# Kernel tuning notes

Hardware: AMD Instinct MI355X
Metric: run time of the kernel (lower is better)

Reference implementation:

```python
import jax, jax.numpy as jnp
import numpy as np

N = 50000        # num nodes
E = 800000       # num edges (before self loops)
F_DIM = 256      # embedding_dim
H = 4            # num_heads
C = 64           # latent_dim
SLOPE = 0.2      # PyG GATConv leaky_relu negative_slope


def setup_inputs() -> dict:
    key = jax.random.key(0)
    ks = jax.random.split(key, 11)
    s = 0.05
    return {
        "x": jax.random.normal(ks[0], (N, F_DIM), jnp.float32),
        "edge_index": jax.random.randint(ks[1], (2, E), 0, N),
        "W1": jax.random.normal(ks[2], (F_DIM, H * C), jnp.float32) * s,
        "a_src1": jax.random.normal(ks[3], (H, C), jnp.float32) * s,
        "a_dst1": jax.random.normal(ks[4], (H, C), jnp.float32) * s,
        "b1": jnp.zeros((H * C,), jnp.float32),
        "W2": jax.random.normal(ks[5], (H * C, F_DIM), jnp.float32) * s,
        "a_src2": jax.random.normal(ks[6], (1, F_DIM), jnp.float32) * s,
        "a_dst2": jax.random.normal(ks[7], (1, F_DIM), jnp.float32) * s,
        "b2": jnp.zeros((F_DIM,), jnp.float32),
    }


def gat_layer(x, src, dst, W, a_src, a_dst, bias, heads, out_ch):
    n = x.shape[0]
    xW = (x @ W).reshape(n, heads, out_ch)              # [N,H,C]
    alpha_s = jnp.sum(xW * a_src, axis=-1)               # [N,H]
    alpha_d = jnp.sum(xW * a_dst, axis=-1)               # [N,H]
    e = jax.nn.leaky_relu(alpha_s[src] + alpha_d[dst], SLOPE)  # [E,H]
    m = jax.ops.segment_max(e, dst, num_segments=n)      # segment-softmax over in-edges
    w = jnp.exp(e - m[dst])
    z = jax.ops.segment_sum(w, dst, num_segments=n)
    alpha = w / z[dst]                                    # [E,H]
    out = jax.ops.segment_sum(xW[src] * alpha[:, :, None], dst, num_segments=n)  # [N,H,C]
    return out.reshape(n, heads * out_ch) + bias          # concat=True


def reference(x, edge_index, W1, a_src1, a_dst1, b1, W2, a_src2, a_dst2, b2):
    loop = jnp.arange(N)  # PyG default add_self_loops=True
    src = jnp.concatenate([edge_index[0], loop])
    dst = jnp.concatenate([edge_index[1], loop])
    h = jax.nn.elu(gat_layer(x, src, dst, W1, a_src1, a_dst1, b1, H, C))
    return gat_layer(h, src, dst, W2, a_src2, a_dst2, b2, 1, F_DIM)
```

## Files before the change

### kernel.cpp

```cpp
#include <hip/hip_runtime.h>
#include <hip/hip_bf16.h>
#include <math.h>

#define N_NODES 50000
#define N_EDGES 800000
#define ETOT    (N_EDGES + N_NODES)
#define FDIM    256
#define SLOPE   0.2f

typedef __bf16    bf16x8 __attribute__((ext_vector_type(8)));
typedef float     f32x4  __attribute__((ext_vector_type(4)));
typedef _Float16  f16x8  __attribute__((ext_vector_type(8)));
typedef _Float16  f16x4  __attribute__((ext_vector_type(4)));

__global__ void count_edges(const int* __restrict__ dst, int* __restrict__ counts) {
    int i = blockIdx.x * blockDim.x + threadIdx.x;
    if (i < N_EDGES) atomicAdd(&counts[dst[i]], 1);
}

__global__ void scan1(const int* __restrict__ counts, int* __restrict__ partial,
                      int* __restrict__ blockSums) {
    __shared__ int wsum[4];
    int b = blockIdx.x, t = threadIdx.x;
    int base = b * 1024;
    int i0 = base + t * 4;
    int v[4];
#pragma unroll
    for (int u = 0; u < 4; u++) { int i = i0 + u; v[u] = (i < N_NODES) ? (counts[i] + 1) : 0; }
    v[1] += v[0]; v[2] += v[1]; v[3] += v[2];
    int lane = t & 63, wid = t >> 6;
    int incl = v[3];
#pragma unroll
    for (int d = 1; d < 64; d <<= 1) {
        int o = __shfl_up(incl, d, 64);
        if (lane >= d) incl += o;
    }
    if (lane == 63) wsum[wid] = incl;
    __syncthreads();
    int woff = 0;
#pragma unroll
    for (int w = 0; w < 4; w++) if (w < wid) woff += wsum[w];
    int texcl = woff + incl - v[3];
#pragma unroll
    for (int u = 0; u < 4; u++) { int i = i0 + u; if (i < N_NODES) partial[i] = texcl + v[u]; }
    if (t == 255) blockSums[b] = woff + incl;
}

__global__ void scan3(const int* __restrict__ partial, const int* __restrict__ blockSums,
                      int* __restrict__ row_ptr, int* __restrict__ cursor) {
    int b = blockIdx.x, t = threadIdx.x;
    __shared__ int s_off;
    if (t < 64) {
        int v = (t < b) ? blockSums[t] : 0;
#pragma unroll
        for (int d = 1; d < 64; d <<= 1) v += __shfl_xor(v, d, 64);
        if (t == 0) s_off = v;
    }
    __syncthreads();
    int off = s_off;
    int base = b * 1024;
#pragma unroll
    for (int u = 0; u < 4; u++) {
        int i = base + t + u * 256;
        if (i < N_NODES) {
            row_ptr[i + 1] = off + partial[i];
            cursor[i]      = off + ((i == base) ? 0 : partial[i - 1]);
        }
    }
    if (b == 0 && t == 0) row_ptr[0] = 0;
}

__global__ void scatter_edges(const int* __restrict__ src, const int* __restrict__ dst,
                              int* __restrict__ cursor, int* __restrict__ col_src) {
    int i = blockIdx.x * blockDim.x + threadIdx.x;
    if (i >= ETOT) return;
    int s, d;
    if (i < N_EDGES) { s = src[i]; d = dst[i]; }
    else             { s = i - N_EDGES; d = s; }
    int p = atomicAdd(&cursor[d], 1);
    col_src[p] = s;
}

__global__ void pack_w2(const float* __restrict__ W1, const float* __restrict__ W2,
                        __bf16* __restrict__ P1, __bf16* __restrict__ P2) {
    int tid = blockIdx.x * 256 + threadIdx.x;
    const float* W = (tid < 65536) ? W1 : W2;
    __bf16* P = (tid < 65536) ? P1 : P2;
    int t = tid & 65535;
    int j    = t & 7;
    int lane = (t >> 3) & 63;
    int nb   = (t >> 9) & 3;
    int w    = (t >> 11) & 3;
    int step = (t >> 13) & 7;
    int col = (w << 6) | (nb << 4) | (lane & 15);
    int k   = (step << 5) | ((lane >> 4) << 3) | j;
    float v = W[(k << 8) | col];
    __bf16 h = (__bf16)v;
    int base = (((((step << 2) | w) << 2) | nb) << 10) | (lane << 3) | j;
    P[base]       = h;
    P[base + 512] = (__bf16)(v - (float)h);
}

template <int HEADS, typename AT>
__global__ __launch_bounds__(256) void gemm_mfma(
        const AT* __restrict__ A, const __bf16* __restrict__ Bpk,
        _Float16* __restrict__ Ch,
        const float* __restrict__ avS, const float* __restrict__ avD,
        float* __restrict__ aS, float* __restrict__ aD, int M) {
    constexpr int LDA = 40;
    constexpr int LDC = 272;
    __shared__ union SMem {
        struct { __bf16 Ah[2][64 * LDA]; __bf16 Al[2][64 * LDA]; } st;
        _Float16 cts[64][LDC];
    } smem;
    __shared__ float sred[2][64][4];

    const int t = threadIdx.x;
    const int w = t >> 6, l = t & 63;
    const int q = l >> 4, c16 = l & 15;
    const int row0 = blockIdx.x * 64;

    const int ar = t >> 2, ak = (t & 3) << 3;
    const bool arow_ok = (row0 + ar) < M;
    const AT* Arow = A + (size_t)(row0 + ar) * 256 + ak;

    f32x4 acc[4][4];
#pragma unroll
    for (int i = 0; i < 4; i++)
#pragma unroll
        for (int j = 0; j < 4; j++) acc[i][j] = (f32x4){0.f, 0.f, 0.f, 0.f};

    float4 pv0 = make_float4(0.f, 0.f, 0.f, 0.f), pv1 = pv0;
    f16x8  pvh = (f16x8){0, 0, 0, 0, 0, 0, 0, 0};
    if (arow_ok) {
        if constexpr (sizeof(AT) == 4) {
            pv0 = *(const float4*)(Arow);
            pv1 = *(const float4*)(Arow + 4);
        } else {
            pvh = *(const f16x8*)(Arow);
        }
    }

    for (int step = 0; step < 8; ++step) {
        const int k0 = step << 5;
        const int buf = step & 1;

        {
            float vv[8];
            if constexpr (sizeof(AT) == 4) {
                vv[0] = pv0.x; vv[1] = pv0.y; vv[2] = pv0.z; vv[3] = pv0.w;
                vv[4] = pv1.x; vv[5] = pv1.y; vv[6] = pv1.z; vv[7] = pv1.w;
            } else {
#pragma unroll
                for (int j = 0; j < 8; j++) vv[j] = (float)pvh[j];
            }
            bf16x8 hv, lv;
#pragma unroll
            for (int j = 0; j < 8; j++) {
                __bf16 hb = (__bf16)vv[j];
                hv[j] = hb;
                lv[j] = (__bf16)(vv[j] - (float)hb);
            }
            *(bf16x8*)(&smem.st.Ah[buf][ar * LDA + ak]) = hv;
            *(bf16x8*)(&smem.st.Al[buf][ar * LDA + ak]) = lv;
        }
        if (step < 7 && arow_ok) {
            if constexpr (sizeof(AT) == 4) {
                pv0 = *(const float4*)(Arow + k0 + 32);
                pv1 = *(const float4*)(Arow + k0 + 36);
            } else {
                pvh = *(const f16x8*)(Arow + k0 + 32);
            }
        }
        const __bf16* Bs = Bpk + ((size_t)((step << 2) | w) << 12);
        bf16x8 bh[4], bl[4];
#pragma unroll
        for (int nb = 0; nb < 4; nb++) {
            bh[nb] = *(const bf16x8*)(Bs + (nb << 10) + (l << 3));
            bl[nb] = *(const bf16x8*)(Bs + (nb << 10) + 512 + (l << 3));
        }
        __syncthreads();

        bf16x8 ah[4], alo[4];
#pragma unroll
        for (int mb = 0; mb < 4; mb++) {
            int off = (c16 + (mb << 4)) * LDA + (q << 3);
            ah[mb]  = *(const bf16x8*)(&smem.st.Ah[buf][off]);
            alo[mb] = *(const bf16x8*)(&smem.st.Al[buf][off]);
        }
#pragma unroll
        for (int mb = 0; mb < 4; mb++)
#pragma unroll
            for (int nb = 0; nb < 4; nb++) {
                acc[mb][nb] = __builtin_amdgcn_mfma_f32_16x16x32_bf16(ah[mb],  bh[nb], acc[mb][nb], 0, 0, 0);
                acc[mb][nb] = __builtin_amdgcn_mfma_f32_16x16x32_bf16(ah[mb],  bl[nb], acc[mb][nb], 0, 0, 0);
                acc[mb][nb] = __builtin_amdgcn_mfma_f32_16x16x32_bf16(alo[mb], bh[nb], acc[mb][nb], 0, 0, 0);
            }
    }
    __syncthreads();

#pragma unroll
    for (int mb = 0; mb < 4; mb++) {
#pragma unroll
        for (int r = 0; r < 4; r++) {
            int row = (mb << 4) + (q << 2) + r;
            float s = 0.f, d = 0.f;
#pragma unroll
            for (int nb = 0; nb < 4; nb++) {
                int col = (w << 6) + (nb << 4) + c16;
                float val = acc[mb][nb][r];
                s = fmaf(val, avS[col], s);
                d = fmaf(val, avD[col], d);
                smem.cts[row][col] = (_Float16)val;
            }
#pragma unroll
            for (int dd = 1; dd < 16; dd <<= 1) {
                s += __shfl_xor(s, dd, 64);
                d += __shfl_xor(d, dd, 64);
            }
            if (c16 == 0) { sred[0][row][w] = s; sred[1][row][w] = d; }
        }
    }
    __syncthreads();

    {
        const int crow = t >> 2;
        const int grow = row0 + crow;
        if (grow < M) {
            _Float16* dstp = Ch + (size_t)grow * 256;
#pragma unroll
            for (int i = 0; i < 8; i++) {
                int col = ((t & 3) << 3) + (i << 5);
                *(f16x8*)(dstp + col) = *(const f16x8*)(&smem.cts[crow][col]);
            }
        }
    }
    if (HEADS == 4) {
        int row = t >> 2, wv = t & 3;
        int v = row0 + row;
        if (v < M) { aS[v * 4 + wv] = sred[0][row][wv]; aD[v * 4 + wv] = sred[1][row][wv]; }
    } else {
        if (t < 64) {
            int v = row0 + t;
            if (v < M) {
                aS[v] = sred[0][t][0] + sred[0][t][1] + sred[0][t][2] + sred[0][t][3];
                aD[v] = sred[1][t][0] + sred[1][t][1] + sred[1][t][2] + sred[1][t][3];
            }
        }
    }
}

template <int HEADS, bool ELU, typename OT>
__global__ __launch_bounds__(256) void gat_aggregate_wave(
        const _Float16* __restrict__ xWh, const float* __restrict__ aS,
        const float* __restrict__ aD, const int* __restrict__ row_ptr,
        const int* __restrict__ col_src, const float* __restrict__ bias,
        OT* __restrict__ out) {
    const int wid  = threadIdx.x >> 6;
    const int lane = threadIdx.x & 63;
    const int v = blockIdx.x * 4 + wid;
    if (v >= N_NODES) return;

    constexpr int CH = 64 / HEADS;
    const int h = (HEADS == 4) ? (lane >> 4) : 0;
    const int q = (HEADS == 4) ? (lane & 15) : lane;

    const int half = lane >> 5;
    const int fl   = lane & 31;
    const int hf   = (HEADS == 4) ? (fl >> 3) : 0;
    const int wbase = (HEADS == 4) ? (hf << 4) : 0;

    const int beg = row_ptr[v], end = row_ptr[v + 1];
    const float adv = aD[v * HEADS + h];

    float acc[8] = {0.f, 0.f, 0.f, 0.f, 0.f, 0.f, 0.f, 0.f};
    float z = 0.f;
    for (int j0 = beg; j0 < end; j0 += CH) {
        const int cnt = min(CH, end - j0);
        int s = 0;
        float wgt = 0.f;
        if (q < cnt) {
            s = col_src[j0 + q];
            float e = aS[s * HEADS + h] + adv;
            e = (e > 0.f) ? e : SLOPE * e;
            wgt = __expf(e);
        }
        z += wgt;
        for (int jj = 0; jj < cnt; jj += 2) {
            const int qm = jj + half;
            const int sl = wbase | qm;
            const int   sj = __shfl(s,   sl, 64);
            const float wj = __shfl(wgt, sl, 64);
            if (qm < cnt) {
                const f16x8 row = *(const f16x8*)(xWh + ((size_t)sj << 8) + (fl << 3));
#pragma unroll
                for (int i = 0; i < 8; i++)
                    acc[i] = fmaf(wj, (float)row[i], acc[i]);
            }
        }
    }
#pragma unroll
    for (int d = 1; d < CH; d <<= 1) z += __shfl_xor(z, d, 64);
    const float zf = (HEADS == 4) ? __shfl(z, hf << 4, 64) : z;

#pragma unroll
    for (int i = 0; i < 8; i++) acc[i] += __shfl_xor(acc[i], 32, 64);

    const float rz = 1.f / zf;
    const int fbase = (fl << 3) + (half << 2);
    const float4 bv = *(const float4*)(bias + fbase);
    float4 o;
    o.x = acc[(half << 2) + 0] * rz + bv.x;
    o.y = acc[(half << 2) + 1] * rz + bv.y;
    o.z = acc[(half << 2) + 2] * rz + bv.z;
    o.w = acc[(half << 2) + 3] * rz + bv.w;
    if (ELU) {
        o.x = (o.x > 0.f) ? o.x : expm1f(o.x);
        o.y = (o.y > 0.f) ? o.y : expm1f(o.y);
        o.z = (o.z > 0.f) ? o.z : expm1f(o.z);
        o.w = (o.w > 0.f) ? o.w : expm1f(o.w);
    }
    if constexpr (sizeof(OT) == 2) {
        f16x4 ov;
        ov[0] = (_Float16)o.x; ov[1] = (_Float16)o.y;
        ov[2] = (_Float16)o.z; ov[3] = (_Float16)o.w;
        *(f16x4*)(out + ((size_t)v << 8) + fbase) = ov;
    } else {
        *(float4*)(out + ((size_t)v << 8) + fbase) = o;
    }
}

extern "C" void kernel_launch(void* const* d_in, const int* in_sizes, int n_in,
                              void* d_out, int out_size, void* d_ws, size_t ws_size,
                              hipStream_t stream) {
    const float* x   = (const float*)d_in[0];
    const int*   ei  = (const int*)d_in[1];
    const float* W1  = (const float*)d_in[2];
    const float* as1 = (const float*)d_in[3];
    const float* ad1 = (const float*)d_in[4];
    const float* b1  = (const float*)d_in[5];
    const float* W2  = (const float*)d_in[6];
    const float* as2 = (const float*)d_in[7];
    const float* ad2 = (const float*)d_in[8];
    const float* b2  = (const float*)d_in[9];
    float* out = (float*)d_out;

    const int* src = ei;
    const int* dst = ei + N_EDGES;

    char* w = (char*)d_ws;
    _Float16* xWh = (_Float16*)w; w += (size_t)N_NODES * 256 * 2;
    _Float16* hh  = (_Float16*)w; w += (size_t)N_NODES * 256 * 2;
    float* aS = (float*)w;  w += (size_t)N_NODES * 4 * 4;
    float* aD = (float*)w;  w += (size_t)N_NODES * 4 * 4;
    int* row_ptr = (int*)w; w += (((size_t)(N_NODES + 1) * 4 + 255) / 256) * 256;
    int* counts  = (int*)w; w += (((size_t)N_NODES * 4 + 255) / 256) * 256;
    int* cursor  = (int*)w; w += (((size_t)N_NODES * 4 + 255) / 256) * 256;
    int* partial = (int*)w; w += (((size_t)N_NODES * 4 + 255) / 256) * 256;
    int* bsums   = (int*)w; w += 256;
    int* col_src = (int*)w; w += (size_t)ETOT * 4;
    __bf16* Wpk1 = (__bf16*)w; w += 131072 * 2;
    __bf16* Wpk2 = (__bf16*)w; w += 131072 * 2;

    int nb = (N_NODES + 1023) / 1024;

    pack_w2<<<512, 256, 0, stream>>>(W1, W2, Wpk1, Wpk2);

    hipMemsetAsync(counts, 0, (size_t)N_NODES * 4, stream);
    count_edges<<<(N_EDGES + 255) / 256, 256, 0, stream>>>(dst, counts);
    scan1<<<nb, 256, 0, stream>>>(counts, partial, bsums);
    scan3<<<nb, 256, 0, stream>>>(partial, bsums, row_ptr, cursor);
    scatter_edges<<<(ETOT + 255) / 256, 256, 0, stream>>>(src, dst, cursor, col_src);

    int gemm_blocks = (N_NODES + 63) / 64;
    int agg_blocks  = (N_NODES + 3) / 4;

    gemm_mfma<4, float><<<gemm_blocks, 256, 0, stream>>>(x, Wpk1, xWh, as1, ad1, aS, aD, N_NODES);
    gat_aggregate_wave<4, true, _Float16><<<agg_blocks, 256, 0, stream>>>(xWh, aS, aD, row_ptr, col_src, b1, hh);

    gemm_mfma<1, _Float16><<<gemm_blocks, 256, 0, stream>>>(hh, Wpk2, xWh, as2, ad2, aS, aD, N_NODES);
    gat_aggregate_wave<1, false, float><<<agg_blocks, 256, 0, stream>>>(xWh, aS, aD, row_ptr, col_src, b2, out);
}
```

Baseline: 299.0 us.

## Fuse CSR build into one cooperative kernel and enlarge GEMM row tile

Replaces the memset, count, two scan and scatter launches with a single cooperative kernel that uses grid-wide syncs between phases, cutting launch overhead and inter-kernel gaps. Separately, the MFMA GEMM now processes 128 rows per block instead of 64, so each B fragment load is reused across twice as many rows. The epilogue is split into two halves so the existing 64-row shared staging buffer still works. Costs are more accumulator registers, possibly lower occupancy, grid.sync overhead, and only 512 blocks doing the atomic-heavy edge phases.

```diff
diff --git a/kernel.cpp b/kernel.cpp
--- a/kernel.cpp
+++ b/kernel.cpp
@@ -1,84 +1,96 @@
 #include <hip/hip_runtime.h>
 #include <hip/hip_bf16.h>
+#include <hip/hip_cooperative_groups.h>
 #include <math.h>
+
+namespace cg = cooperative_groups;
 
 #define N_NODES 50000
 #define N_EDGES 800000
 #define ETOT    (N_EDGES + N_NODES)
 #define FDIM    256
 #define SLOPE   0.2f
+#define CSR_BLOCKS 512
+#define SCAN_NB  ((N_NODES + 1023) / 1024)
 
 typedef __bf16    bf16x8 __attribute__((ext_vector_type(8)));
 typedef float     f32x4  __attribute__((ext_vector_type(4)));
 typedef _Float16  f16x8  __attribute__((ext_vector_type(8)));
 typedef _Float16  f16x4  __attribute__((ext_vector_type(4)));
 
-__global__ void count_edges(const int* __restrict__ dst, int* __restrict__ counts) {
-    int i = blockIdx.x * blockDim.x + threadIdx.x;
-    if (i < N_EDGES) atomicAdd(&counts[dst[i]], 1);
-}
-
-__global__ void scan1(const int* __restrict__ counts, int* __restrict__ partial,
-                      int* __restrict__ blockSums) {
+__global__ void __launch_bounds__(256) fused_csr(
+        const int* __restrict__ src, const int* __restrict__ dst,
+        int* __restrict__ counts, int* __restrict__ partial,
+        int* __restrict__ bsums, int* __restrict__ row_ptr,
+        int* __restrict__ cursor, int* __restrict__ col_src) {
+    cg::grid_group grid = cg::this_grid();
     __shared__ int wsum[4];
-    int b = blockIdx.x, t = threadIdx.x;
-    int base = b * 1024;
-    int i0 = base + t * 4;
-    int v[4];
-#pragma unroll
-    for (int u = 0; u < 4; u++) { int i = i0 + u; v[u] = (i < N_NODES) ? (counts[i] + 1) : 0; }
-    v[1] += v[0]; v[2] += v[1]; v[3] += v[2];
-    int lane = t & 63, wid = t >> 6;
-    int incl = v[3];
-#pragma unroll
-    for (int d = 1; d < 64; d <<= 1) {
-        int o = __shfl_up(incl, d, 64);
-        if (lane >= d) incl += o;
-    }
-    if (lane == 63) wsum[wid] = incl;
-    __syncthreads();
-    int woff = 0;
-#pragma unroll
-    for (int w = 0; w < 4; w++) if (w < wid) woff += wsum[w];
-    int texcl = woff + incl - v[3];
-#pragma unroll
-    for (int u = 0; u < 4; u++) { int i = i0 + u; if (i < N_NODES) partial[i] = texcl + v[u]; }
-    if (t == 255) blockSums[b] = woff + incl;
-}
-
-__global__ void scan3(const int* __restrict__ partial, const int* __restrict__ blockSums,
-                      int* __restrict__ row_ptr, int* __restrict__ cursor) {
-    int b = blockIdx.x, t = threadIdx.x;
     __shared__ int s_off;
-    if (t < 64) {
-        int v = (t < b) ? blockSums[t] : 0;
-#pragma unroll
-        for (int d = 1; d < 64; d <<= 1) v += __shfl_xor(v, d, 64);
-        if (t == 0) s_off = v;
-    }
-    __syncthreads();
-    int off = s_off;
-    int base = b * 1024;
-#pragma unroll
-    for (int u = 0; u < 4; u++) {
-        int i = base + t + u * 256;
-        if (i < N_NODES) {
-            row_ptr[i + 1] = off + partial[i];
-            cursor[i]      = off + ((i == base) ? 0 : partial[i - 1]);
-        }
-    }
-    if (b == 0 && t == 0) row_ptr[0] = 0;
-}
-
-__global__ void scatter_edges(const int* __restrict__ src, const int* __restrict__ dst,
-                              int* __restrict__ cursor, int* __restrict__ col_src) {
-    int i = blockIdx.x * blockDim.x + threadIdx.x;
-    if (i >= ETOT) return;
-    int s, d;
-    if (i < N_EDGES) { s = src[i]; d = dst[i]; }
-    else             { s = i - N_EDGES; d = s; }
-    int p = atomicAdd(&cursor[d], 1);
-    col_src[p] = s;
+    const int t = threadIdx.x, b = blockIdx.x;
+    const int gtid = b * 256 + t;
+    const int gsz = gridDim.x * 256;
+
+    for (int i = gtid; i < N_NODES; i += gsz) counts[i] = 0;
+    grid.sync();
+
+    for (int i = gtid; i < N_EDGES; i += gsz) atomicAdd(&counts[dst[i]], 1);
+    grid.sync();
+
+    if (b < SCAN_NB) {
+        int base = b * 1024;
+        int i0 = base + t * 4;
+        int v[4];
+#pragma unroll
+        for (int u = 0; u < 4; u++) { int i = i0 + u; v[u] = (i < N_NODES) ? (counts[i] + 1) : 0; }
+        v[1] += v[0]; v[2] += v[1]; v[3] += v[2];
+        int lane = t & 63, wid = t >> 6;
+        int incl = v[3];
+#pragma unroll
+        for (int d = 1; d < 64; d <<= 1) {
+            int o = __shfl_up(incl, d, 64);
+            if (lane >= d) incl += o;
+        }
+        if (lane == 63) wsum[wid] = incl;
+        __syncthreads();
+        int woff = 0;
+#pragma unroll
+        for (int w = 0; w < 4; w++) if (w < wid) woff += wsum[w];
+        int texcl = woff + incl - v[3];
+#pragma unroll
+        for (int u = 0; u < 4; u++) { int i = i0 + u; if (i < N_NODES) partial[i] = texcl + v[u]; }
+        if (t == 255) bsums[b] = woff + incl;
+    }
+    grid.sync();
+
+    if (b < SCAN_NB) {
+        if (t < 64) {
+            int v = (t < b) ? bsums[t] : 0;
+#pragma unroll
+            for (int d = 1; d < 64; d <<= 1) v += __shfl_xor(v, d, 64);
+            if (t == 0) s_off = v;
+        }
+        __syncthreads();
+        int off = s_off;
+        int base = b * 1024;
+#pragma unroll
+        for (int u = 0; u < 4; u++) {
+            int i = base + t + u * 256;
+            if (i < N_NODES) {
+                row_ptr[i + 1] = off + partial[i];
+                cursor[i]      = off + ((i == base) ? 0 : partial[i - 1]);
+            }
+        }
+        if (b == 0 && t == 0) row_ptr[0] = 0;
+    }
+    grid.sync();
+
+    for (int i = gtid; i < ETOT; i += gsz) {
+        int s, d;
+        if (i < N_EDGES) { s = src[i]; d = dst[i]; }
+        else             { s = i - N_EDGES; d = s; }
+        int p = atomicAdd(&cursor[d], 1);
+        col_src[p] = s;
+    }
 }
 
 __global__ void pack_w2(const float* __restrict__ W1, const float* __restrict__ W2,
@@ -110,7 +122,7 @@
     constexpr int LDA = 40;
     constexpr int LDC = 272;
     __shared__ union SMem {
-        struct { __bf16 Ah[2][64 * LDA]; __bf16 Al[2][64 * LDA]; } st;
+        struct { __bf16 Ah[2][128 * LDA]; __bf16 Al[2][128 * LDA]; } st;
         _Float16 cts[64][LDC];
     } smem;
     __shared__ float sred[2][64][4];
@@ -118,26 +130,30 @@
     const int t = threadIdx.x;
     const int w = t >> 6, l = t & 63;
     const int q = l >> 4, c16 = l & 15;
-    const int row0 = blockIdx.x * 64;
-
-    const int ar = t >> 2, ak = (t & 3) << 3;
+    const int row0 = blockIdx.x * 128;
+
+    const int ar = t >> 1, ak = (t & 1) << 4;
     const bool arow_ok = (row0 + ar) < M;
     const AT* Arow = A + (size_t)(row0 + ar) * 256 + ak;
 
-    f32x4 acc[4][4];
-#pragma unroll
-    for (int i = 0; i < 4; i++)
+    f32x4 acc[8][4];
+#pragma unroll
+    for (int i = 0; i < 8; i++)
 #pragma unroll
         for (int j = 0; j < 4; j++) acc[i][j] = (f32x4){0.f, 0.f, 0.f, 0.f};
 
-    float4 pv0 = make_float4(0.f, 0.f, 0.f, 0.f), pv1 = pv0;
-    f16x8  pvh = (f16x8){0, 0, 0, 0, 0, 0, 0, 0};
+    float4 pv[4];
+    f16x8  pvh[2];
+#pragma unroll
+    for (int i = 0; i < 4; i++) pv[i] = make_float4(0.f, 0.f, 0.f, 0.f);
+    pvh[0] = (f16x8){0,0,0,0,0,0,0,0}; pvh[1] = pvh[0];
     if (arow_ok) {
         if constexpr (sizeof(AT) == 4) {
-            pv0 = *(const float4*)(Arow);
-            pv1 = *(const float4*)(Arow + 4);
+#pragma unroll
+            for (int i = 0; i < 4; i++) pv[i] = *(const float4*)(Arow + (i << 2));
         } else {
-            pvh = *(const f16x8*)(Arow);
+            pvh[0] = *(const f16x8*)(Arow);
+            pvh[1] = *(const f16x8*)(Arow + 8);
         }
     }
 
@@ -146,30 +162,36 @@
         const int buf = step & 1;
 
         {
-            float vv[8];
+            float vv[16];
             if constexpr (sizeof(AT) == 4) {
-                vv[0] = pv0.x; vv[1] = pv0.y; vv[2] = pv0.z; vv[3] = pv0.w;
-                vv[4] = pv1.x; vv[5] = pv1.y; vv[6] = pv1.z; vv[7] = pv1.w;
+#pragma unroll
+                for (int i = 0; i < 4; i++) {
+                    vv[i * 4 + 0] = pv[i].x; vv[i * 4 + 1] = pv[i].y;
+                    vv[i * 4 + 2] = pv[i].z; vv[i * 4 + 3] = pv[i].w;
+                }
             } else {
 #pragma unroll
-                for (int j = 0; j < 8; j++) vv[j] = (float)pvh[j];
-            }
-            bf16x8 hv, lv;
-#pragma unroll
-            for (int j = 0; j < 8; j++) {
-                __bf16 hb = (__bf16)vv[j];
-                hv[j] = hb;
-                lv[j] = (__bf16)(vv[j] - (float)hb);
-            }
-            *(bf16x8*)(&smem.st.Ah[buf][ar * LDA + ak]) = hv;
-            *(bf16x8*)(&smem.st.Al[buf][ar * LDA + ak]) = lv;
+                for (int i = 0; i < 16; i++) vv[i] = (float)pvh[i >> 3][i & 7];
+            }
+            bf16x8 hv[2], lv[2];
+#pragma unroll
+            for (int i = 0; i < 16; i++) {
+                __bf16 hb = (__bf16)vv[i];
+                hv[i >> 3][i & 7] = hb;
+                lv[i >> 3][i & 7] = (__bf16)(vv[i] - (float)hb);
+            }
+            *(bf16x8*)(&smem.st.Ah[buf][ar * LDA + ak])     = hv[0];
+            *(bf16x8*)(&smem.st.Ah[buf][ar * LDA + ak + 8]) = hv[1];
+            *(bf16x8*)(&smem.st.Al[buf][ar * LDA + ak])     = lv[0];
+            *(bf16x8*)(&smem.st.Al[buf][ar * LDA + ak + 8]) = lv[1];
         }
         if (step < 7 && arow_ok) {
             if constexpr (sizeof(AT) == 4) {
-                pv0 = *(const float4*)(Arow + k0 + 32);
-                pv1 = *(const float4*)(Arow + k0 + 36);
+#pragma unroll
+                for (int i = 0; i < 4; i++) pv[i] = *(const float4*)(Arow + k0 + 32 + (i << 2));
             } else {
-                pvh = *(const f16x8*)(Arow + k0 + 32);
+                pvh[0] = *(const f16x8*)(Arow + k0 + 32);
+                pvh[1] = *(const f16x8*)(Arow + k0 + 40);
             }
         }
         const __bf16* Bs = Bpk + ((size_t)((step << 2) | w) << 12);
@@ -181,70 +203,71 @@
         }
         __syncthreads();
 
-        bf16x8 ah[4], alo[4];
-#pragma unroll
-        for (int mb = 0; mb < 4; mb++) {
+#pragma unroll
+        for (int mb = 0; mb < 8; mb++) {
             int off = (c16 + (mb << 4)) * LDA + (q << 3);
-            ah[mb]  = *(const bf16x8*)(&smem.st.Ah[buf][off]);
-            alo[mb] = *(const bf16x8*)(&smem.st.Al[buf][off]);
-        }
-#pragma unroll
-        for (int mb = 0; mb < 4; mb++)
+            bf16x8 ah  = *(const bf16x8*)(&smem.st.Ah[buf][off]);
+            bf16x8 alo = *(const bf16x8*)(&smem.st.Al[buf][off]);
 #pragma unroll
             for (int nb = 0; nb < 4; nb++) {
-                acc[mb][nb] = __builtin_amdgcn_mfma_f32_16x16x32_bf16(ah[mb],  bh[nb], acc[mb][nb], 0, 0, 0);
-                acc[mb][nb] = __builtin_amdgcn_mfma_f32_16x16x32_bf16(ah[mb],  bl[nb], acc[mb][nb], 0, 0, 0);
-                acc[mb][nb] = __builtin_amdgcn_mfma_f32_16x16x32_bf16(alo[mb], bh[nb], acc[mb][nb], 0, 0, 0);
-            }
-    }
-    __syncthreads();
-
-#pragma unroll
-    for (int mb = 0; mb < 4; mb++) {
-#pragma unroll
-        for (int r = 0; r < 4; r++) {
-            int row = (mb << 4) + (q << 2) + r;
-            float s = 0.f, d = 0.f;
-#pragma unroll
-            for (int nb = 0; nb < 4; nb++) {
-                int col = (w << 6) + (nb << 4) + c16;
-                float val = acc[mb][nb][r];
-                s = fmaf(val, avS[col], s);
-                d = fmaf(val, avD[col], d);
-                smem.cts[row][col] = (_Float16)val;
-            }
-#pragma unroll
-            for (int dd = 1; dd < 16; dd <<= 1) {
-                s += __shfl_xor(s, dd, 64);
-                d += __shfl_xor(d, dd, 64);
-            }
-            if (c16 == 0) { sred[0][row][w] = s; sred[1][row][w] = d; }
-        }
-    }
-    __syncthreads();
-
-    {
-        const int crow = t >> 2;
-        const int grow = row0 + crow;
-        if (grow < M) {
-            _Float16* dstp = Ch + (size_t)grow * 256;
-#pragma unroll
-            for (int i = 0; i < 8; i++) {
-                int col = ((t & 3) << 3) + (i << 5);
-                *(f16x8*)(dstp + col) = *(const f16x8*)(&smem.cts[crow][col]);
-            }
-        }
-    }
-    if (HEADS == 4) {
-        int row = t >> 2, wv = t & 3;
-        int v = row0 + row;
-        if (v < M) { aS[v * 4 + wv] = sred[0][row][wv]; aD[v * 4 + wv] = sred[1][row][wv]; }
-    } else {
-        if (t < 64) {
-            int v = row0 + t;
-            if (v < M) {
-                aS[v] = sred[0][t][0] + sred[0][t][1] + sred[0][t][2] + sred[0][t][3];
-                aD[v] = sred[1][t][0] + sred[1][t][1] + sred[1][t][2] + sred[1][t][3];
+                acc[mb][nb] = __builtin_amdgcn_mfma_f32_16x16x32_bf16(ah,  bh[nb], acc[mb][nb], 0, 0, 0);
+                acc[mb][nb] = __builtin_amdgcn_mfma_f32_16x16x32_bf16(ah,  bl[nb], acc[mb][nb], 0, 0, 0);
+                acc[mb][nb] = __builtin_amdgcn_mfma_f32_16x16x32_bf16(alo, bh[nb], acc[mb][nb], 0, 0, 0);
+            }
+        }
+    }
+
+#pragma unroll
+    for (int half = 0; half < 2; ++half) {
+        __syncthreads();
+#pragma unroll
+        for (int mbl = 0; mbl < 4; mbl++) {
+            const int mb = (half << 2) | mbl;
+#pragma unroll
+            for (int r = 0; r < 4; r++) {
+                int row = (mbl << 4) + (q << 2) + r;
+                float s = 0.f, d = 0.f;
+#pragma unroll
+                for (int nb = 0; nb < 4; nb++) {
+                    int col = (w << 6) + (nb << 4) + c16;
+                    float val = acc[mb][nb][r];
+                    s = fmaf(val, avS[col], s);
+                    d = fmaf(val, avD[col], d);
+                    smem.cts[row][col] = (_Float16)val;
+                }
+#pragma unroll
+                for (int dd = 1; dd < 16; dd <<= 1) {
+                    s += __shfl_xor(s, dd, 64);
+                    d += __shfl_xor(d, dd, 64);
+                }
+                if (c16 == 0) { sred[0][row][w] = s; sred[1][row][w] = d; }
+            }
+        }
+        __syncthreads();
+
+        {
+            const int crow = t >> 2;
+            const int grow = row0 + (half << 6) + crow;
+            if (grow < M) {
+                _Float16* dstp = Ch + (size_t)grow * 256;
+#pragma unroll
+                for (int i = 0; i < 8; i++) {
+                    int col = ((t & 3) << 3) + (i << 5);
+                    *(f16x8*)(dstp + col) = *(const f16x8*)(&smem.cts[crow][col]);
+                }
+            }
+        }
+        if (HEADS == 4) {
+            int row = t >> 2, wv = t & 3;
+            int v = row0 + (half << 6) + row;
+            if (v < M) { aS[v * 4 + wv] = sred[0][row][wv]; aD[v * 4 + wv] = sred[1][row][wv]; }
+        } else {
+            if (t < 64) {
+                int v = row0 + (half << 6) + t;
+                if (v < M) {
+                    aS[v] = sred[0][t][0] + sred[0][t][1] + sred[0][t][2] + sred[0][t][3];
+                    aD[v] = sred[1][t][0] + sred[1][t][1] + sred[1][t][2] + sred[1][t][3];
+                }
             }
         }
     }
@@ -362,17 +385,16 @@
     __bf16* Wpk1 = (__bf16*)w; w += 131072 * 2;
     __bf16* Wpk2 = (__bf16*)w; w += 131072 * 2;
 
-    int nb = (N_NODES + 1023) / 1024;
+    {
+        void* args[] = {(void*)&src, (void*)&dst, (void*)&counts, (void*)&partial,
+                        (void*)&bsums, (void*)&row_ptr, (void*)&cursor, (void*)&col_src};
+        hipLaunchCooperativeKernel((void*)fused_csr, dim3(CSR_BLOCKS), dim3(256),
+                                   args, 0, stream);
+    }
 
     pack_w2<<<512, 256, 0, stream>>>(W1, W2, Wpk1, Wpk2);
 
-    hipMemsetAsync(counts, 0, (size_t)N_NODES * 4, stream);
-    count_edges<<<(N_EDGES + 255) / 256, 256, 0, stream>>>(dst, counts);
-    scan1<<<nb, 256, 0, stream>>>(counts, partial, bsums);
-    scan3<<<nb, 256, 0, stream>>>(partial, bsums, row_ptr, cursor);
-    scatter_edges<<<(ETOT + 255) / 256, 256, 0, stream>>>(src, dst, cursor, col_src);
-
-    int gemm_blocks = (N_NODES + 63) / 64;
+    int gemm_blocks = (N_NODES + 127) / 128;
     int agg_blocks  = (N_NODES + 3) / 4;
 
     gemm_mfma<4, float><<<gemm_blocks, 256, 0, stream>>>(x, Wpk1, xWh, as1, ad1, aS, aD, N_NODES);
```

New measurement: 502.6 us. 68.1% more time.
